# Performance work log

Measured on AMD Instinct MI355X. Metric: run time of the kernel, lower is better.

Reference implementation:

```python
import jax, jax.numpy as jnp
import numpy as np

N = 50000      # n_points (== n_support, non-strided)
H = 32         # neighbors per point
IN_F = 128
OUT_F = 256
MID = OUT_F // 4   # bottleneck width = 64
K = 15         # kernel points
RADIUS = 2.0
KP_EXTENT = 1.2 * RADIUS / 5.0  # config.KP_extent * radius / density_parameter
EPS = 1e-6
SLOPE = 0.1


def _wvar(k, size):
    # weight_variable: normal(scale=sqrt(2/size[-1])), zeroed outside 2*std
    std = np.sqrt(2.0 / size[-1])
    w = jax.random.normal(k, size, jnp.float32) * std
    return jnp.where(jnp.abs(w) > 2.0 * std, 0.0, w)


def setup_inputs():
    key = jax.random.key(0)
    ks = jax.random.split(key, 12)
    query_points = jax.random.uniform(ks[0], (N, 3), jnp.float32)
    support_points = query_points  # non-strided: same cloud
    neighbors_indices = jax.random.randint(ks[1], (N, H), 0, N, jnp.int32)
    features = jax.random.normal(ks[2], (N, IN_F), jnp.float32)
    kp = (jax.random.uniform(ks[3], (K, 3), jnp.float32) * 2.0 - 1.0) * (0.66 * KP_EXTENT)
    kernel_points = kp.at[0].set(0.0)  # fixed_kernel_points='center'
    w1 = _wvar(ks[4], (IN_F, MID))
    kw = _wvar(ks[5], (K, MID, MID))
    w3 = _wvar(ks[6], (MID, OUT_F))
    ws = _wvar(ks[7], (IN_F, OUT_F))
    def bnp(k, c):
        k1, k2 = jax.random.split(k)
        g = jax.random.uniform(k1, (c,), jnp.float32, 0.75, 1.25)
        b = jax.random.normal(k2, (c,), jnp.float32) * 0.1
        return g, b
    g1, b1 = bnp(ks[8], MID)
    g2, b2 = bnp(ks[9], MID)
    g3, b3 = bnp(ks[10], OUT_F)
    gs, bs = bnp(ks[11], OUT_F)
    return dict(query_points=query_points, support_points=support_points,
                neighbors_indices=neighbors_indices, features=features,
                kernel_points=kernel_points, w1=w1, g1=g1, b1=b1,
                kw=kw, g2=g2, b2=b2, w3=w3, g3=g3, b3=b3, ws=ws, gs=gs, bs=bs)


def _bn(x, g, b):
    # BatchNorm1d in training mode: batch statistics over points, biased var
    m = jnp.mean(x, 0)
    v = jnp.var(x, 0)
    return g * (x - m) * jax.lax.rsqrt(v + EPS) + b


def _lrelu(x):
    return jnp.where(x >= 0, x, SLOPE * x)


def _unary(x, w, g, b):
    return _lrelu(_bn(x @ w, g, b))


def _kpconv(q, s, inds, f, kp, kw):
    # pad support with a far shadow point and features with a zero row (faithful to KPConv)
    s_pad = jnp.concatenate([s, jnp.full((1, 3), 1e6, s.dtype)], 0)
    f_pad = jnp.concatenate([f, jnp.zeros((1, f.shape[1]), f.dtype)], 0)
    neigh = s_pad[inds]                        # [n,h,3] gather
    d = neigh - q[:, None, :]                  # [n,h,3]
    sq = jnp.sum((d[:, :, None, :] - kp[None, None, :, :]) ** 2, -1)  # [n,h,K]
    dist = jnp.sqrt(jnp.maximum(sq, 1e-12))
    infl = jnp.maximum(0.0, 1.0 - dist / KP_EXTENT)   # 'linear' KP_influence
    nf = f_pad[inds]                           # [n,h,d] gather
    wf = jnp.einsum('nhk,nhd->nkd', infl, nf)  # aggregate over neighbors
    return jnp.einsum('nkd,kdo->no', wf, kw)   # 'sum' aggregation over kernel pts


def reference(query_points, support_points, neighbors_indices, features, kernel_points,
              w1, g1, b1, kw, g2, b2, w3, g3, b3, ws, gs, bs):
    x = _unary(features, w1, g1, b1)                                     # conv1
    x = _lrelu(_bn(_kpconv(query_points, support_points, neighbors_indices,
                           x, kernel_points, kw), g2, b2))               # conv2 (KPConv)
    x = _unary(x, w3, g3, b3)                                            # conv3
    sc = _unary(features, ws, gs, bs)                                    # shortcut (non-strided)
    return _lrelu(sc + x)
```

## Files before the change

kernel.cpp:

```cpp
#include <hip/hip_runtime.h>

#define NPTS 50000
#define HN 32
#define INF1 128
#define OUTF3 256
#define MIDF 64
#define KP 15
#define EPSV 1e-6f
#define SLOPE 0.1f
#define KPE 0.48f
#define INVN (1.f / 50000.f)

typedef __attribute__((ext_vector_type(8))) short short8;
typedef __attribute__((ext_vector_type(4))) float float4v;
typedef unsigned short ushort;
typedef unsigned long long ull;

__device__ inline ushort f2bf(float f) {
    union { float f; unsigned u; } v; v.f = f;
    unsigned r = v.u + 0x7fff + ((v.u >> 16) & 1);
    return (ushort)(r >> 16);
}
__device__ inline float bf2f(ushort u) {
    union { unsigned u; float f; } v; v.u = ((unsigned)u) << 16;
    return v.f;
}

__device__ inline void repack_one(const float* W, ushort* Wp, int K, int N, int lid) {
    int l  = lid & 63;
    int NT = N / 16;
    int nt = (lid >> 6) % NT;
    int s  = lid / (64 * NT);
    int n  = nt * 16 + (l & 15);
    int k0 = s * 32 + ((l >> 4) & 3) * 8;
#pragma unroll
    for (int j = 0; j < 8; j++)
        Wp[lid * 8 + j] = f2bf(W[(k0 + j) * N + n]);
}

__global__ __launch_bounds__(256)
void k_repack_all(const float* __restrict__ w1, const float* __restrict__ wsw,
                  ushort* __restrict__ wpC,
                  const float* __restrict__ kw, ushort* __restrict__ wpk,
                  const float* __restrict__ w3, ushort* __restrict__ wp3) {
    int id = blockIdx.x * 256 + threadIdx.x;
    if (id < 5120) {
        int l  = id & 63;
        int nt = (id >> 6) % 20;
        int s  = id / 1280;
        int n  = nt * 16 + (l & 15);
        int k0 = s * 32 + ((l >> 4) & 3) * 8;
#pragma unroll
        for (int j = 0; j < 8; j++) {
            float v = (n < 64) ? w1[(k0 + j) * 64 + n] : wsw[(k0 + j) * 256 + (n - 64)];
            wpC[id * 8 + j] = f2bf(v);
        }
    } else if (id < 12800) {
        repack_one(kw, wpk, KP * MIDF, MIDF, id - 5120);
    } else if (id < 14848) {
        repack_one(w3, wp3, MIDF, OUTF3, id - 12800);
    }
}

__global__ __launch_bounds__(256)
void k_conv1sc(const float* __restrict__ feat, const ushort* __restrict__ WpC,
               ushort* __restrict__ x1raw, ushort* __restrict__ scb,
               float* __restrict__ Sa1, float* __restrict__ Sq1,
               float* __restrict__ SaS, float* __restrict__ SqS, int M) {
    constexpr int KSTEPS = 4, NT = 20;
    __shared__ float sred[320], qred[320];
    int t = threadIdx.x;
    int w = t >> 6, l = t & 63;
    int dl = l & 15, q4 = l >> 4;

    for (int c = t; c < 320; c += 256) { sred[c] = 0.f; qred[c] = 0.f; }
    __syncthreads();

    int m0 = blockIdx.x * 64 + w * 16;
    int row = m0 + dl;
    long arow = (row < M) ? row : (M - 1);
    const float* ap0 = feat + arow * INF1 + q4 * 8;
    const short8* Bp = (const short8*)WpC + l;

    float4v acc[NT];
#pragma unroll
    for (int j = 0; j < NT; j++) acc[j] = (float4v){0.f, 0.f, 0.f, 0.f};

#pragma unroll
    for (int s = 0; s < KSTEPS; s++) {
        const float* ap = ap0 + s * 32;
        float4 a0 = *(const float4*)(ap);
        float4 a1 = *(const float4*)(ap + 4);
        union { short8 v; ushort u[8]; } au;
        au.u[0] = f2bf(a0.x); au.u[1] = f2bf(a0.y); au.u[2] = f2bf(a0.z); au.u[3] = f2bf(a0.w);
        au.u[4] = f2bf(a1.x); au.u[5] = f2bf(a1.y); au.u[6] = f2bf(a1.z); au.u[7] = f2bf(a1.w);
#pragma unroll
        for (int j = 0; j < NT; j++) {
            short8 bf = Bp[(s * NT + j) * 64];
            acc[j] = __builtin_amdgcn_mfma_f32_16x16x32_bf16(au.v, bf, acc[j], 0, 0, 0);
        }
    }

    int rb = q4 * 4;
#pragma unroll
    for (int r = 0; r < 4; r++) {
        int rr = m0 + rb + r;
        if (rr < M) {
#pragma unroll
            for (int j = 0; j < NT; j++) {
                int c = j * 16 + dl;
                ushort v = f2bf(acc[j][r]);
                if (c < 64) x1raw[(long)rr * 64 + c] = v;
                else        scb[(long)rr * 256 + (c - 64)] = v;
            }
        }
    }

#pragma unroll
    for (int j = 0; j < NT; j++) {
        float s = 0.f, q = 0.f;
#pragma unroll
        for (int r = 0; r < 4; r++) {
            float v = ((m0 + rb + r) < M) ? acc[j][r] : 0.f;
            s += v; q += v * v;
        }
        s += __shfl_xor(s, 16); s += __shfl_xor(s, 32);
        q += __shfl_xor(q, 16); q += __shfl_xor(q, 32);
        if (q4 == 0) {
            atomicAdd(&sred[j * 16 + dl], s);
            atomicAdd(&qred[j * 16 + dl], q);
        }
    }
    __syncthreads();
    for (int c = t; c < 320; c += 256) {
        if (c < 64) { atomicAdd(&Sa1[c], sred[c]); atomicAdd(&Sq1[c], qred[c]); }
        else        { atomicAdd(&SaS[c - 64], sred[c]); atomicAdd(&SqS[c - 64], qred[c]); }
    }
}

__global__ __launch_bounds__(256)
void k_conv3(const ushort* __restrict__ x2raw, const ushort* __restrict__ Wp,
             ushort* __restrict__ x3b,
             const float* __restrict__ Sa2, const float* __restrict__ Sq2,
             const float* __restrict__ g2, const float* __restrict__ b2,
             float* __restrict__ Sa3, float* __restrict__ Sq3, int M) {
    constexpr int NT = 16;
    __shared__ float sred[256], qred[256];
    __shared__ float scs[64], shs[64];
    int t = threadIdx.x;
    int w = t >> 6, l = t & 63;
    int dl = l & 15, q4 = l >> 4;

    if (t < 64) {
        float m = Sa2[t] * INVN;
        float v = Sq2[t] * INVN - m * m;
        float s = g2[t] * rsqrtf(v + EPSV);
        scs[t] = s; shs[t] = b2[t] - s * m;
    }
    if (t < 256) { sred[t] = 0.f; qred[t] = 0.f; }
    __syncthreads();

    int m0 = blockIdx.x * 64 + w * 16;
    int row = m0 + dl;
    long arow = (row < M) ? row : (M - 1);
    const ushort* ap0 = x2raw + arow * MIDF + q4 * 8;
    const short8* Bp = (const short8*)Wp + l;

    float4v acc[NT];
#pragma unroll
    for (int j = 0; j < NT; j++) acc[j] = (float4v){0.f, 0.f, 0.f, 0.f};

#pragma unroll
    for (int s = 0; s < 2; s++) {
        union { short8 v; ushort u[8]; } raw;
        raw.v = *(const short8*)(ap0 + s * 32);
        const float* scv = &scs[s * 32 + q4 * 8];
        const float* shv = &shs[s * 32 + q4 * 8];
        union { short8 v; ushort u[8]; } au;
#pragma unroll
        for (int e = 0; e < 8; e++) {
            float f = bf2f(raw.u[e]) * scv[e] + shv[e];
            f = (f >= 0.f) ? f : SLOPE * f;
            au.u[e] = f2bf(f);
        }
#pragma unroll
        for (int j = 0; j < NT; j++) {
            short8 bf = Bp[(s * NT + j) * 64];
            acc[j] = __builtin_amdgcn_mfma_f32_16x16x32_bf16(au.v, bf, acc[j], 0, 0, 0);
        }
    }

    int rb = q4 * 4;
#pragma unroll
    for (int r = 0; r < 4; r++) {
        int rr = m0 + rb + r;
        if (rr < M) {
#pragma unroll
            for (int j = 0; j < NT; j++)
                x3b[(long)rr * 256 + j * 16 + dl] = f2bf(acc[j][r]);
        }
    }

#pragma unroll
    for (int j = 0; j < NT; j++) {
        float s = 0.f, q = 0.f;
#pragma unroll
        for (int r = 0; r < 4; r++) {
            float v = ((m0 + rb + r) < M) ? acc[j][r] : 0.f;
            s += v; q += v * v;
        }
        s += __shfl_xor(s, 16); s += __shfl_xor(s, 32);
        q += __shfl_xor(q, 16); q += __shfl_xor(q, 32);
        if (q4 == 0) {
            atomicAdd(&sred[j * 16 + dl], s);
            atomicAdd(&qred[j * 16 + dl], q);
        }
    }
    __syncthreads();
    if (t < 256) {
        atomicAdd(&Sa3[t], sred[t]);
        atomicAdd(&Sq3[t], qred[t]);
    }
}

__global__ __launch_bounds__(256)
void k_bnx(const ushort* __restrict__ X, ushort* __restrict__ Y,
           const float* __restrict__ Sa, const float* __restrict__ Sq,
           const float* __restrict__ g, const float* __restrict__ b) {
    __shared__ float sc[64], sh[64];
    int t = threadIdx.x;
    if (t < 64) {
        float m = Sa[t] * INVN;
        float v = Sq[t] * INVN - m * m;
        float s = g[t] * rsqrtf(v + EPSV);
        sc[t] = s; sh[t] = b[t] - s * m;
    }
    __syncthreads();
    long i = (long)(blockIdx.x * 256 + t) * 4;
    ull vin = *(const ull*)(X + i);
    int c0 = (int)(i & 63);
    ull vout = 0;
#pragma unroll
    for (int j = 0; j < 4; j++) {
        float f = bf2f((ushort)((vin >> (16 * j)) & 0xffff));
        float v = f * sc[c0 + j] + sh[c0 + j];
        v = (v >= 0.f) ? v : SLOPE * v;
        vout |= ((ull)f2bf(v)) << (16 * j);
    }
    *(ull*)(Y + i) = vout;
}

__global__ __launch_bounds__(256)
void k_kpconv(const float* __restrict__ qpts, const float* __restrict__ spts,
              const int* __restrict__ nbr, const ushort* __restrict__ x1b,
              const float* __restrict__ kpp, const ushort* __restrict__ kwp,
              ushort* __restrict__ y, float* __restrict__ Sa, float* __restrict__ Sq) {
    __shared__ __align__(16) ushort wfs[16][968];
    __shared__ __align__(16) ushort fst[4][HN][68];
    __shared__ float posd[4][3][HN];
    __shared__ int   sidx[4][HN];

    int t = threadIdx.x;
    int w = t >> 6, l = t & 63;
    int dl = l & 15, q4 = l >> 4;
    int hrow = l >> 3, seg = l & 7;

    int kmin = (dl < 15) ? dl : 14;
    float kx = kpp[kmin * 3 + 0], ky = kpp[kmin * 3 + 1], kz = kpp[kmin * 3 + 2];

    for (int pp = 0; pp < 4; pp++) {
        int p = w * 4 + pp;
        int n = blockIdx.x * 16 + p;

        if (l < HN) {
            int idx = nbr[n * HN + l];
            sidx[w][l] = idx;
            float qx = qpts[n * 3 + 0], qy = qpts[n * 3 + 1], qz = qpts[n * 3 + 2];
            posd[w][0][l] = spts[idx * 3 + 0] - qx;
            posd[w][1][l] = spts[idx * 3 + 1] - qy;
            posd[w][2][l] = spts[idx * 3 + 2] - qz;
        }

#pragma unroll
        for (int c = 0; c < 4; c++) {
            int h = c * 8 + hrow;
            long r = (long)sidx[w][h] * MIDF + seg * 8;
            uint2 d0 = *(const uint2*)(x1b + r);
            uint2 d1 = *(const uint2*)(x1b + r + 4);
            *(uint2*)&fst[w][h][seg * 8]     = d0;
            *(uint2*)&fst[w][h][seg * 8 + 4] = d1;
        }

        union { short8 v; ushort u[8]; } afr;
#pragma unroll
        for (int j = 0; j < 8; j++) {
            int h = q4 * 8 + j;
            float ex = posd[w][0][h] - kx;
            float ey = posd[w][1][h] - ky;
            float ez = posd[w][2][h] - kz;
            float sq = ex * ex + ey * ey + ez * ez;
            float dist = sqrtf(fmaxf(sq, 1e-12f));
            float inf = fmaxf(0.f, 1.f - dist * (1.f / KPE));
            afr.u[j] = (dl < 15) ? f2bf(inf) : (ushort)0;
        }

        union { short8 v; ushort u[8]; } bfr[4];
#pragma unroll
        for (int nt = 0; nt < 4; nt++)
#pragma unroll
            for (int j = 0; j < 8; j++)
                bfr[nt].u[j] = fst[w][q4 * 8 + j][nt * 16 + dl];

        float4v wfacc[4];
#pragma unroll
        for (int nt = 0; nt < 4; nt++)
            wfacc[nt] = __builtin_amdgcn_mfma_f32_16x16x32_bf16(
                afr.v, bfr[nt].v, (float4v){0.f, 0.f, 0.f, 0.f}, 0, 0, 0);

#pragma unroll
        for (int ntx = 0; ntx < 4; ntx++) {
            int nt = (ntx + q4) & 3;
#pragma unroll
            for (int r = 0; r < 4; r++) {
                int k = q4 * 4 + r;
                if (k < 15)
                    wfs[p][k * 64 + nt * 16 + dl] = f2bf(wfacc[nt][r]);
            }
        }
    }
    __syncthreads();

    float4v acc = (float4v){0.f, 0.f, 0.f, 0.f};
    const ushort* arow = &wfs[dl][0] + q4 * 8;
    const short8* Bp = (const short8*)kwp + l;
#pragma unroll 6
    for (int s = 0; s < 30; s++) {
        short8 af = *(const short8*)(arow + s * 32);
        short8 bf = Bp[(s * 4 + w) * 64];
        acc = __builtin_amdgcn_mfma_f32_16x16x32_bf16(af, bf, acc, 0, 0, 0);
    }

    int o = w * 16 + dl;
    float s = 0.f, q = 0.f;
#pragma unroll
    for (int r = 0; r < 4; r++) {
        float v = acc[r];
        y[(long)(blockIdx.x * 16 + q4 * 4 + r) * MIDF + o] = f2bf(v);
        s += v; q += v * v;
    }
    s += __shfl_xor(s, 16); s += __shfl_xor(s, 32);
    q += __shfl_xor(q, 16); q += __shfl_xor(q, 32);
    if (q4 == 0) {
        atomicAdd(&Sa[o], s);
        atomicAdd(&Sq[o], q);
    }
}

__global__ __launch_bounds__(256)
void k_final(const ushort* __restrict__ x3b, const ushort* __restrict__ scb,
             float* __restrict__ out,
             const float* __restrict__ a3, const float* __restrict__ q3,
             const float* __restrict__ g3, const float* __restrict__ b3,
             const float* __restrict__ aS, const float* __restrict__ qS,
             const float* __restrict__ gs, const float* __restrict__ bs) {
    __shared__ float s3[256], h3[256], sS[256], hS[256];
    int t = threadIdx.x;
    {
        float m = a3[t] * INVN;
        float v = q3[t] * INVN - m * m;
        float s = g3[t] * rsqrtf(v + EPSV);
        s3[t] = s; h3[t] = b3[t] - s * m;
        m = aS[t] * INVN;
        v = qS[t] * INVN - m * m;
        s = gs[t] * rsqrtf(v + EPSV);
        sS[t] = s; hS[t] = bs[t] - s * m;
    }
    __syncthreads();
    long i = (long)(blockIdx.x * 256 + t) * 4;
    int c0 = (int)(i & 255);
    ull va = *(const ull*)(x3b + i);
    ull vb = *(const ull*)(scb + i);
    float r[4];
#pragma unroll
    for (int j = 0; j < 4; j++) {
        int c = c0 + j;
        float x = bf2f((ushort)((va >> (16 * j)) & 0xffff)) * s3[c] + h3[c];
        x = (x >= 0.f) ? x : SLOPE * x;
        float sc = bf2f((ushort)((vb >> (16 * j)) & 0xffff)) * sS[c] + hS[c];
        sc = (sc >= 0.f) ? sc : SLOPE * sc;
        float v = x + sc;
        r[j] = (v >= 0.f) ? v : SLOPE * v;
    }
    *(float4*)(out + i) = (float4){r[0], r[1], r[2], r[3]};
}

extern "C" void kernel_launch(void* const* d_in, const int* in_sizes, int n_in,
                              void* d_out, int out_size, void* d_ws, size_t ws_size,
                              hipStream_t stream) {
    const float* qp   = (const float*)d_in[0];
    const float* sp   = (const float*)d_in[1];
    const int*   nbr  = (const int*)d_in[2];
    const float* feat = (const float*)d_in[3];
    const float* kpp  = (const float*)d_in[4];
    const float* w1   = (const float*)d_in[5];
    const float* g1   = (const float*)d_in[6];
    const float* b1   = (const float*)d_in[7];
    const float* kw   = (const float*)d_in[8];
    const float* g2   = (const float*)d_in[9];
    const float* b2   = (const float*)d_in[10];
    const float* w3   = (const float*)d_in[11];
    const float* g3   = (const float*)d_in[12];
    const float* b3   = (const float*)d_in[13];
    const float* wsw  = (const float*)d_in[14];
    const float* gs   = (const float*)d_in[15];
    const float* bs   = (const float*)d_in[16];
    float* out = (float*)d_out;

    char* base = (char*)d_ws;
    ushort* x1raw = (ushort*)(base + 0);
    ushort* x1b   = (ushort*)(base + 6400000);
    ushort* x2raw = (ushort*)(base + 12800000);
    ushort* x3b   = (ushort*)(base + 19200000);
    ushort* scb   = (ushort*)(base + 44800000);
    ushort* wpC   = (ushort*)(base + 70400000);
    ushort* wpk   = (ushort*)(base + 70481920);
    ushort* wp3   = (ushort*)(base + 70604800);
    float*  st    = (float*)(base + 70637568);
    float* acc1 = st,       *q1 = st + 64;
    float* acc2 = st + 128, *q2 = st + 192;
    float* acc3 = st + 256, *q3 = st + 512;
    float* accS = st + 768, *qS = st + 1024;

    hipMemsetAsync(st, 0, 1280 * sizeof(float), stream);

    k_repack_all<<<58, 256, 0, stream>>>(w1, wsw, wpC, kw, wpk, w3, wp3);

    k_conv1sc<<<782, 256, 0, stream>>>(feat, wpC, x1raw, scb, acc1, q1, accS, qS, NPTS);
    k_bnx<<<3125, 256, 0, stream>>>(x1raw, x1b, acc1, q1, g1, b1);

    k_kpconv<<<NPTS / 16, 256, 0, stream>>>(qp, sp, nbr, x1b, kpp, wpk, x2raw, acc2, q2);

    k_conv3<<<782, 256, 0, stream>>>(x2raw, wp3, x3b, acc2, q2, g2, b2, acc3, q3, NPTS);

    k_final<<<12500, 256, 0, stream>>>(x3b, scb, out, acc3, q3, g3, b3, accS, qS, gs, bs);
}
```

Before: 326.7 us.

## Interleave x1 channel layout so KPConv gathers neighbor features directly into MFMA fragments

conv1 now writes x1 in a permuted channel layout where each lane's four 16-channel-strided values sit together in one 8-byte word. The KPConv kernel reads neighbor features straight from global memory into registers and builds B fragments with byte permutes, which removes the shared-memory staging tile and its transposed reads. The kernel-point weights are repacked with a d-major, k-padded-to-16 ordering so the stored intermediate and the second MFMA loop use 32 aligned steps instead of 30. conv1 and conv3 also split their accumulators into two halves to lower register pressure. The trade-off is more scattered 8-byte global gathers and some wasted MFMA work on the zero padding.

```diff
diff --git a/kernel.cpp b/kernel.cpp
--- a/kernel.cpp
+++ b/kernel.cpp
@@ -26,17 +26,6 @@
     return v.f;
 }
 
-__device__ inline void repack_one(const float* W, ushort* Wp, int K, int N, int lid) {
-    int l  = lid & 63;
-    int NT = N / 16;
-    int nt = (lid >> 6) % NT;
-    int s  = lid / (64 * NT);
-    int n  = nt * 16 + (l & 15);
-    int k0 = s * 32 + ((l >> 4) & 3) * 8;
-#pragma unroll
-    for (int j = 0; j < 8; j++)
-        Wp[lid * 8 + j] = f2bf(W[(k0 + j) * N + n]);
-}
 
 __global__ __launch_bounds__(256)
 void k_repack_all(const float* __restrict__ w1, const float* __restrict__ wsw,
@@ -45,20 +34,36 @@
                   const float* __restrict__ w3, ushort* __restrict__ wp3) {
     int id = blockIdx.x * 256 + threadIdx.x;
     if (id < 5120) {
-        int l  = id & 63;
-        int nt = (id >> 6) % 20;
-        int s  = id / 1280;
-        int n  = nt * 16 + (l & 15);
+        int l = id & 63;
+        int nt = (id >> 6) % 20, s = id / 1280;
+        int n = nt * 16 + (l & 15);
         int k0 = s * 32 + ((l >> 4) & 3) * 8;
 #pragma unroll
         for (int j = 0; j < 8; j++) {
             float v = (n < 64) ? w1[(k0 + j) * 64 + n] : wsw[(k0 + j) * 256 + (n - 64)];
             wpC[id * 8 + j] = f2bf(v);
         }
-    } else if (id < 12800) {
-        repack_one(kw, wpk, KP * MIDF, MIDF, id - 5120);
-    } else if (id < 14848) {
-        repack_one(w3, wp3, MIDF, OUTF3, id - 12800);
+    } else if (id < 13312) {
+        int id2 = id - 5120;
+        int l2 = id2 & 63;
+        int nt = (id2 >> 6) & 3, s = id2 >> 8;
+        int n = nt * 16 + (l2 & 15);
+        int kd0 = s * 32 + ((l2 >> 4) & 3) * 8;
+#pragma unroll
+        for (int j = 0; j < 8; j++) {
+            int kd = kd0 + j, d = kd >> 4, kk = kd & 15;
+            float v = (kk < KP) ? kw[kk * 4096 + d * 64 + n] : 0.f;
+            wpk[id2 * 8 + j] = f2bf(v);
+        }
+    } else if (id < 15360) {
+        int id3 = id - 13312;
+        int l3 = id3 & 63;
+        int nt = (id3 >> 6) % 16, s = id3 / 1024;
+        int n = nt * 16 + (l3 & 15);
+        int k0 = s * 32 + ((l3 >> 4) & 3) * 8;
+#pragma unroll
+        for (int j = 0; j < 8; j++)
+            wp3[id3 * 8 + j] = f2bf(w3[(k0 + j) * 256 + n]);
     }
 }
 
@@ -67,7 +72,6 @@
                ushort* __restrict__ x1raw, ushort* __restrict__ scb,
                float* __restrict__ Sa1, float* __restrict__ Sq1,
                float* __restrict__ SaS, float* __restrict__ SqS, int M) {
-    constexpr int KSTEPS = 4, NT = 20;
     __shared__ float sred[320], qred[320];
     int t = threadIdx.x;
     int w = t >> 6, l = t & 63;
@@ -80,146 +84,70 @@
     int row = m0 + dl;
     long arow = (row < M) ? row : (M - 1);
     const float* ap0 = feat + arow * INF1 + q4 * 8;
-    const short8* Bp = (const short8*)WpC + l;
-
-    float4v acc[NT];
-#pragma unroll
-    for (int j = 0; j < NT; j++) acc[j] = (float4v){0.f, 0.f, 0.f, 0.f};
-
-#pragma unroll
-    for (int s = 0; s < KSTEPS; s++) {
-        const float* ap = ap0 + s * 32;
-        float4 a0 = *(const float4*)(ap);
-        float4 a1 = *(const float4*)(ap + 4);
+    short8 afr[4];
+#pragma unroll
+    for (int s = 0; s < 4; s++) {
+        float4 a0 = *(const float4*)(ap0 + s * 32);
+        float4 a1 = *(const float4*)(ap0 + s * 32 + 4);
         union { short8 v; ushort u[8]; } au;
         au.u[0] = f2bf(a0.x); au.u[1] = f2bf(a0.y); au.u[2] = f2bf(a0.z); au.u[3] = f2bf(a0.w);
         au.u[4] = f2bf(a1.x); au.u[5] = f2bf(a1.y); au.u[6] = f2bf(a1.z); au.u[7] = f2bf(a1.w);
-#pragma unroll
-        for (int j = 0; j < NT; j++) {
-            short8 bf = Bp[(s * NT + j) * 64];
-            acc[j] = __builtin_amdgcn_mfma_f32_16x16x32_bf16(au.v, bf, acc[j], 0, 0, 0);
-        }
-    }
-
+        afr[s] = au.v;
+    }
+    const short8* Bp = (const short8*)WpC + l;
     int rb = q4 * 4;
 #pragma unroll
-    for (int r = 0; r < 4; r++) {
-        int rr = m0 + rb + r;
-        if (rr < M) {
-#pragma unroll
-            for (int j = 0; j < NT; j++) {
-                int c = j * 16 + dl;
-                ushort v = f2bf(acc[j][r]);
-                if (c < 64) x1raw[(long)rr * 64 + c] = v;
-                else        scb[(long)rr * 256 + (c - 64)] = v;
-            }
-        }
-    }
-
-#pragma unroll
-    for (int j = 0; j < NT; j++) {
-        float s = 0.f, q = 0.f;
+    for (int half = 0; half < 2; half++) {
+        float4v acc[10];
+#pragma unroll
+        for (int j = 0; j < 10; j++) acc[j] = (float4v){0.f, 0.f, 0.f, 0.f};
+#pragma unroll
+        for (int s = 0; s < 4; s++)
+#pragma unroll
+            for (int j = 0; j < 10; j++) {
+                short8 bf = Bp[(s * 20 + half * 10 + j) * 64];
+                acc[j] = __builtin_amdgcn_mfma_f32_16x16x32_bf16(afr[s], bf, acc[j], 0, 0, 0);
+            }
 #pragma unroll
         for (int r = 0; r < 4; r++) {
-            float v = ((m0 + rb + r) < M) ? acc[j][r] : 0.f;
-            s += v; q += v * v;
-        }
-        s += __shfl_xor(s, 16); s += __shfl_xor(s, 32);
-        q += __shfl_xor(q, 16); q += __shfl_xor(q, 32);
-        if (q4 == 0) {
-            atomicAdd(&sred[j * 16 + dl], s);
-            atomicAdd(&qred[j * 16 + dl], q);
+            int rr = m0 + rb + r;
+            if (rr < M) {
+                if (half == 0) {
+                    ull pk = 0;
+#pragma unroll
+                    for (int j = 0; j < 4; j++)
+                        pk |= ((ull)f2bf(acc[j][r])) << (16 * j);
+                    *(ull*)(x1raw + (long)rr * 64 + 4 * dl) = pk;
+#pragma unroll
+                    for (int j = 4; j < 10; j++)
+                        scb[(long)rr * 256 + (j * 16 + dl - 64)] = f2bf(acc[j][r]);
+                } else {
+#pragma unroll
+                    for (int j = 0; j < 10; j++)
+                        scb[(long)rr * 256 + ((10 + j) * 16 + dl - 64)] = f2bf(acc[j][r]);
+                }
+            }
+        }
+#pragma unroll
+        for (int j = 0; j < 10; j++) {
+            float s = 0.f, q = 0.f;
+#pragma unroll
+            for (int r = 0; r < 4; r++) {
+                float v = ((m0 + rb + r) < M) ? acc[j][r] : 0.f;
+                s += v; q += v * v;
+            }
+            s += __shfl_xor(s, 16); s += __shfl_xor(s, 32);
+            q += __shfl_xor(q, 16); q += __shfl_xor(q, 32);
+            if (q4 == 0) {
+                atomicAdd(&sred[(half * 10 + j) * 16 + dl], s);
+                atomicAdd(&qred[(half * 10 + j) * 16 + dl], q);
+            }
         }
     }
     __syncthreads();
     for (int c = t; c < 320; c += 256) {
         if (c < 64) { atomicAdd(&Sa1[c], sred[c]); atomicAdd(&Sq1[c], qred[c]); }
         else        { atomicAdd(&SaS[c - 64], sred[c]); atomicAdd(&SqS[c - 64], qred[c]); }
-    }
-}
-
-__global__ __launch_bounds__(256)
-void k_conv3(const ushort* __restrict__ x2raw, const ushort* __restrict__ Wp,
-             ushort* __restrict__ x3b,
-             const float* __restrict__ Sa2, const float* __restrict__ Sq2,
-             const float* __restrict__ g2, const float* __restrict__ b2,
-             float* __restrict__ Sa3, float* __restrict__ Sq3, int M) {
-    constexpr int NT = 16;
-    __shared__ float sred[256], qred[256];
-    __shared__ float scs[64], shs[64];
-    int t = threadIdx.x;
-    int w = t >> 6, l = t & 63;
-    int dl = l & 15, q4 = l >> 4;
-
-    if (t < 64) {
-        float m = Sa2[t] * INVN;
-        float v = Sq2[t] * INVN - m * m;
-        float s = g2[t] * rsqrtf(v + EPSV);
-        scs[t] = s; shs[t] = b2[t] - s * m;
-    }
-    if (t < 256) { sred[t] = 0.f; qred[t] = 0.f; }
-    __syncthreads();
-
-    int m0 = blockIdx.x * 64 + w * 16;
-    int row = m0 + dl;
-    long arow = (row < M) ? row : (M - 1);
-    const ushort* ap0 = x2raw + arow * MIDF + q4 * 8;
-    const short8* Bp = (const short8*)Wp + l;
-
-    float4v acc[NT];
-#pragma unroll
-    for (int j = 0; j < NT; j++) acc[j] = (float4v){0.f, 0.f, 0.f, 0.f};
-
-#pragma unroll
-    for (int s = 0; s < 2; s++) {
-        union { short8 v; ushort u[8]; } raw;
-        raw.v = *(const short8*)(ap0 + s * 32);
-        const float* scv = &scs[s * 32 + q4 * 8];
-        const float* shv = &shs[s * 32 + q4 * 8];
-        union { short8 v; ushort u[8]; } au;
-#pragma unroll
-        for (int e = 0; e < 8; e++) {
-            float f = bf2f(raw.u[e]) * scv[e] + shv[e];
-            f = (f >= 0.f) ? f : SLOPE * f;
-            au.u[e] = f2bf(f);
-        }
-#pragma unroll
-        for (int j = 0; j < NT; j++) {
-            short8 bf = Bp[(s * NT + j) * 64];
-            acc[j] = __builtin_amdgcn_mfma_f32_16x16x32_bf16(au.v, bf, acc[j], 0, 0, 0);
-        }
-    }
-
-    int rb = q4 * 4;
-#pragma unroll
-    for (int r = 0; r < 4; r++) {
-        int rr = m0 + rb + r;
-        if (rr < M) {
-#pragma unroll
-            for (int j = 0; j < NT; j++)
-                x3b[(long)rr * 256 + j * 16 + dl] = f2bf(acc[j][r]);
-        }
-    }
-
-#pragma unroll
-    for (int j = 0; j < NT; j++) {
-        float s = 0.f, q = 0.f;
-#pragma unroll
-        for (int r = 0; r < 4; r++) {
-            float v = ((m0 + rb + r) < M) ? acc[j][r] : 0.f;
-            s += v; q += v * v;
-        }
-        s += __shfl_xor(s, 16); s += __shfl_xor(s, 32);
-        q += __shfl_xor(q, 16); q += __shfl_xor(q, 32);
-        if (q4 == 0) {
-            atomicAdd(&sred[j * 16 + dl], s);
-            atomicAdd(&qred[j * 16 + dl], q);
-        }
-    }
-    __syncthreads();
-    if (t < 256) {
-        atomicAdd(&Sa3[t], sred[t]);
-        atomicAdd(&Sq3[t], qred[t]);
     }
 }
 
@@ -236,18 +164,20 @@
         sc[t] = s; sh[t] = b[t] - s * m;
     }
     __syncthreads();
-    long i = (long)(blockIdx.x * 256 + t) * 4;
-    ull vin = *(const ull*)(X + i);
-    int c0 = (int)(i & 63);
+    int i = blockIdx.x * 256 + t;
+    long base = (long)i * 4;
+    int dlp = i & 15;
+    ull vin = *(const ull*)(X + base);
     ull vout = 0;
 #pragma unroll
     for (int j = 0; j < 4; j++) {
+        int c = j * 16 + dlp;
         float f = bf2f((ushort)((vin >> (16 * j)) & 0xffff));
-        float v = f * sc[c0 + j] + sh[c0 + j];
+        float v = f * sc[c] + sh[c];
         v = (v >= 0.f) ? v : SLOPE * v;
         vout |= ((ull)f2bf(v)) << (16 * j);
     }
-    *(ull*)(Y + i) = vout;
+    *(ull*)(Y + base) = vout;
 }
 
 __global__ __launch_bounds__(256)
@@ -255,17 +185,15 @@
               const int* __restrict__ nbr, const ushort* __restrict__ x1b,
               const float* __restrict__ kpp, const ushort* __restrict__ kwp,
               ushort* __restrict__ y, float* __restrict__ Sa, float* __restrict__ Sq) {
-    __shared__ __align__(16) ushort wfs[16][968];
-    __shared__ __align__(16) ushort fst[4][HN][68];
+    __shared__ __align__(16) ushort wfs[16][1032];
     __shared__ float posd[4][3][HN];
     __shared__ int   sidx[4][HN];
 
     int t = threadIdx.x;
     int w = t >> 6, l = t & 63;
     int dl = l & 15, q4 = l >> 4;
-    int hrow = l >> 3, seg = l & 7;
-
-    int kmin = (dl < 15) ? dl : 14;
+
+    int kmin = (dl < KP) ? dl : (KP - 1);
     float kx = kpp[kmin * 3 + 0], ky = kpp[kmin * 3 + 1], kz = kpp[kmin * 3 + 2];
 
     for (int pp = 0; pp < 4; pp++) {
@@ -281,17 +209,15 @@
             posd[w][2][l] = spts[idx * 3 + 2] - qz;
         }
 
-#pragma unroll
-        for (int c = 0; c < 4; c++) {
-            int h = c * 8 + hrow;
-            long r = (long)sidx[w][h] * MIDF + seg * 8;
-            uint2 d0 = *(const uint2*)(x1b + r);
-            uint2 d1 = *(const uint2*)(x1b + r + 4);
-            *(uint2*)&fst[w][h][seg * 8]     = d0;
-            *(uint2*)&fst[w][h][seg * 8 + 4] = d1;
-        }
-
-        union { short8 v; ushort u[8]; } afr;
+        uint2 rj[8];
+#pragma unroll
+        for (int j = 0; j < 8; j++) {
+            const ull* pj = (const ull*)(x1b + (long)sidx[w][q4 * 8 + j] * MIDF + 4 * dl);
+            union { ull u; uint2 d; } tmp; tmp.u = *pj;
+            rj[j] = tmp.d;
+        }
+
+        union { short8 v; ushort u8[8]; } afr;
 #pragma unroll
         for (int j = 0; j < 8; j++) {
             int h = q4 * 8 + j;
@@ -301,31 +227,35 @@
             float sq = ex * ex + ey * ey + ez * ez;
             float dist = sqrtf(fmaxf(sq, 1e-12f));
             float inf = fmaxf(0.f, 1.f - dist * (1.f / KPE));
-            afr.u[j] = (dl < 15) ? f2bf(inf) : (ushort)0;
-        }
-
-        union { short8 v; ushort u[8]; } bfr[4];
+            afr.u8[j] = (dl < KP) ? f2bf(inf) : (ushort)0;
+        }
+
+        union { short8 v; unsigned d[4]; } bfr[4];
+#pragma unroll
+        for (int dj = 0; dj < 4; dj++) {
+            unsigned a_lo = rj[2 * dj].x, b_lo = rj[2 * dj + 1].x;
+            unsigned a_hi = rj[2 * dj].y, b_hi = rj[2 * dj + 1].y;
+            bfr[0].d[dj] = __builtin_amdgcn_perm(b_lo, a_lo, 0x05040100u);
+            bfr[1].d[dj] = __builtin_amdgcn_perm(b_lo, a_lo, 0x07060302u);
+            bfr[2].d[dj] = __builtin_amdgcn_perm(b_hi, a_hi, 0x05040100u);
+            bfr[3].d[dj] = __builtin_amdgcn_perm(b_hi, a_hi, 0x07060302u);
+        }
+
+        float4v wfa[4];
 #pragma unroll
         for (int nt = 0; nt < 4; nt++)
-#pragma unroll
-            for (int j = 0; j < 8; j++)
-                bfr[nt].u[j] = fst[w][q4 * 8 + j][nt * 16 + dl];
-
-        float4v wfacc[4];
-#pragma unroll
-        for (int nt = 0; nt < 4; nt++)
-            wfacc[nt] = __builtin_amdgcn_mfma_f32_16x16x32_bf16(
+            wfa[nt] = __builtin_amdgcn_mfma_f32_16x16x32_bf16(
                 afr.v, bfr[nt].v, (float4v){0.f, 0.f, 0.f, 0.f}, 0, 0, 0);
 
 #pragma unroll
-        for (int ntx = 0; ntx < 4; ntx++) {
-            int nt = (ntx + q4) & 3;
+        for (int nt = 0; nt < 4; nt++) {
+            ull pk = 0;
 #pragma unroll
             for (int r = 0; r < 4; r++) {
-                int k = q4 * 4 + r;
-                if (k < 15)
-                    wfs[p][k * 64 + nt * 16 + dl] = f2bf(wfacc[nt][r]);
-            }
+                ushort hv = ((q4 * 4 + r) < KP) ? f2bf(wfa[nt][r]) : (ushort)0;
+                pk |= ((ull)hv) << (16 * r);
+            }
+            *(ull*)(&wfs[p][(nt * 16 + dl) * 16 + q4 * 4]) = pk;
         }
     }
     __syncthreads();
@@ -333,8 +263,8 @@
     float4v acc = (float4v){0.f, 0.f, 0.f, 0.f};
     const ushort* arow = &wfs[dl][0] + q4 * 8;
     const short8* Bp = (const short8*)kwp + l;
-#pragma unroll 6
-    for (int s = 0; s < 30; s++) {
+#pragma unroll 8
+    for (int s = 0; s < 32; s++) {
         short8 af = *(const short8*)(arow + s * 32);
         short8 bf = Bp[(s * 4 + w) * 64];
         acc = __builtin_amdgcn_mfma_f32_16x16x32_bf16(af, bf, acc, 0, 0, 0);
@@ -354,6 +284,89 @@
         atomicAdd(&Sa[o], s);
         atomicAdd(&Sq[o], q);
     }
+}
+
+__global__ __launch_bounds__(256)
+void k_conv3(const ushort* __restrict__ x2raw, const ushort* __restrict__ Wp,
+             ushort* __restrict__ x3b,
+             const float* __restrict__ Sa2, const float* __restrict__ Sq2,
+             const float* __restrict__ g2, const float* __restrict__ b2,
+             float* __restrict__ Sa3, float* __restrict__ Sq3, int M) {
+    __shared__ float sred[256], qred[256];
+    __shared__ float scs[64], shs[64];
+    int t = threadIdx.x;
+    int w = t >> 6, l = t & 63;
+    int dl = l & 15, q4 = l >> 4;
+
+    if (t < 64) {
+        float m = Sa2[t] * INVN;
+        float v = Sq2[t] * INVN - m * m;
+        float s = g2[t] * rsqrtf(v + EPSV);
+        scs[t] = s; shs[t] = b2[t] - s * m;
+    }
+    sred[t] = 0.f; qred[t] = 0.f;
+    __syncthreads();
+
+    int m0 = blockIdx.x * 64 + w * 16;
+    int row = m0 + dl;
+    long arow = (row < M) ? row : (M - 1);
+    const ushort* ap0 = x2raw + arow * MIDF + q4 * 8;
+    short8 au2[2];
+#pragma unroll
+    for (int s = 0; s < 2; s++) {
+        union { short8 v; ushort u[8]; } raw, cv;
+        raw.v = *(const short8*)(ap0 + s * 32);
+#pragma unroll
+        for (int e = 0; e < 8; e++) {
+            int d = s * 32 + q4 * 8 + e;
+            float f = bf2f(raw.u[e]) * scs[d] + shs[d];
+            f = (f >= 0.f) ? f : SLOPE * f;
+            cv.u[e] = f2bf(f);
+        }
+        au2[s] = cv.v;
+    }
+    const short8* Bp = (const short8*)Wp + l;
+    int rb = q4 * 4;
+#pragma unroll
+    for (int half = 0; half < 2; half++) {
+        float4v acc[8];
+#pragma unroll
+        for (int j = 0; j < 8; j++) acc[j] = (float4v){0.f, 0.f, 0.f, 0.f};
+#pragma unroll
+        for (int s = 0; s < 2; s++)
+#pragma unroll
+            for (int j = 0; j < 8; j++) {
+                short8 bf = Bp[(s * 16 + half * 8 + j) * 64];
+                acc[j] = __builtin_amdgcn_mfma_f32_16x16x32_bf16(au2[s], bf, acc[j], 0, 0, 0);
+            }
+#pragma unroll
+        for (int r = 0; r < 4; r++) {
+            int rr = m0 + rb + r;
+            if (rr < M) {
+#pragma unroll
+                for (int j = 0; j < 8; j++)
+                    x3b[(long)rr * 256 + (half * 8 + j) * 16 + dl] = f2bf(acc[j][r]);
+            }
+        }
+#pragma unroll
+        for (int j = 0; j < 8; j++) {
+            float s = 0.f, q = 0.f;
+#pragma unroll
+            for (int r = 0; r < 4; r++) {
+                float v = ((m0 + rb + r) < M) ? acc[j][r] : 0.f;
+                s += v; q += v * v;
+            }
+            s += __shfl_xor(s, 16); s += __shfl_xor(s, 32);
+            q += __shfl_xor(q, 16); q += __shfl_xor(q, 32);
+            if (q4 == 0) {
+                atomicAdd(&sred[(half * 8 + j) * 16 + dl], s);
+                atomicAdd(&qred[(half * 8 + j) * 16 + dl], q);
+            }
+        }
+    }
+    __syncthreads();
+    atomicAdd(&Sa3[t], sred[t]);
+    atomicAdd(&Sq3[t], qred[t]);
 }
 
 __global__ __launch_bounds__(256)
@@ -424,8 +437,8 @@
     ushort* scb   = (ushort*)(base + 44800000);
     ushort* wpC   = (ushort*)(base + 70400000);
     ushort* wpk   = (ushort*)(base + 70481920);
-    ushort* wp3   = (ushort*)(base + 70604800);
-    float*  st    = (float*)(base + 70637568);
+    ushort* wp3   = (ushort*)(base + 70612992);
+    float*  st    = (float*)(base + 70645760);
     float* acc1 = st,       *q1 = st + 64;
     float* acc2 = st + 128, *q2 = st + 192;
     float* acc3 = st + 256, *q3 = st + 512;
@@ -433,7 +446,7 @@
 
     hipMemsetAsync(st, 0, 1280 * sizeof(float), stream);
 
-    k_repack_all<<<58, 256, 0, stream>>>(w1, wsw, wpC, kw, wpk, w3, wp3);
+    k_repack_all<<<60, 256, 0, stream>>>(w1, wsw, wpC, kw, wpk, w3, wp3);
 
     k_conv1sc<<<782, 256, 0, stream>>>(feat, wpC, x1raw, scb, acc1, q1, accS, qS, NPTS);
     k_bnx<<<3125, 256, 0, stream>>>(x1raw, x1b, acc1, q1, g1, b1);
```

After: 301.1 us. -7.8%, faster.
